# Optimization experiments

Hardware: AMD Instinct MI355X
Metric: run time of the kernel (lower is better)

The kernel has to match this reference:

```python
import jax, jax.numpy as jnp
import numpy as np

D_MODEL = 2048
N_HEADS = 16
D_HEAD = D_MODEL // N_HEADS
B, S = 4, 2048


def setup_inputs() -> dict:
    key = jax.random.key(0)
    ks = jax.random.split(key, 5)
    scale = 1.0 / np.sqrt(D_MODEL)
    return {
        "x": jax.random.normal(ks[0], (B, S, D_MODEL), dtype=jnp.float32),
        "w_qkv": jax.random.normal(ks[1], (D_MODEL, 3 * D_MODEL), dtype=jnp.float32) * scale,
        "b_qkv": jax.random.normal(ks[2], (3 * D_MODEL,), dtype=jnp.float32) * 0.01,
        "w_out": jax.random.normal(ks[3], (D_MODEL, D_MODEL), dtype=jnp.float32) * scale,
        "b_out": jax.random.normal(ks[4], (D_MODEL,), dtype=jnp.float32) * 0.01,
    }


def reference(x, w_qkv, b_qkv, w_out, b_out):
    b, s, d = x.shape
    qkv = x @ w_qkv + b_qkv                      # [b, s, 3d]
    q, k, v = jnp.split(qkv, 3, axis=-1)
    # [b, h, s, dh]
    q = q.reshape(b, s, N_HEADS, D_HEAD).transpose(0, 2, 1, 3)
    k = k.reshape(b, s, N_HEADS, D_HEAD).transpose(0, 2, 1, 3)
    v = v.reshape(b, s, N_HEADS, D_HEAD).transpose(0, 2, 1, 3)
    # past_kv is None -> s_past == s
    scale = 1.0 / np.sqrt(D_HEAD).astype(np.float32)
    scores = jnp.einsum("bhqd,bhkd->bhqk", q, k) * scale  # [b, h, s, s]
    # causal mask: disallow j > i (diagonal = 1 + s_past - s = 1)
    causal = jnp.tril(jnp.ones((s, s), dtype=bool))
    scores = jnp.where(causal, scores, jnp.float32(-jnp.inf))
    attn = jax.nn.softmax(scores, axis=-1)
    out = jnp.einsum("bhqk,bhkd->bhqd", attn, v)          # [b, h, s, dh]
    out = out.transpose(0, 2, 1, 3).reshape(b, s, d)
    out = out @ w_out + b_out
    return out, k, v
```

## Files before the change

### kernel.cpp

```cpp
#include <hip/hip_runtime.h>
#include <hip/hip_bf16.h>
#include <cstdint>

typedef unsigned short u16;
typedef unsigned int u32;
typedef __attribute__((ext_vector_type(4))) float f32x4;
typedef __attribute__((ext_vector_type(8))) __bf16 bf16x8;

#define DEVFN static __device__ __forceinline__

constexpr int Bb = 4, S = 2048, Dm = 2048, H = 16, DH = 128;
constexpr int M  = Bb * S;
constexpr int N3 = 3 * Dm;
constexpr float ATTN_SCALE = 0.088388347648318447f;
constexpr float LOG2E = 1.4426950408889634f;

DEVFN u16 f2bf(float f) {
  union { float f; u32 u; } v; v.f = f;
  u32 u = v.u;
  return (u16)((u + 0x7fffu + ((u >> 16) & 1u)) >> 16);
}

DEVFN void async16(const void* g, void* l) {
  __builtin_amdgcn_global_load_lds(
      (__attribute__((address_space(1))) unsigned int*)(g),
      (__attribute__((address_space(3))) unsigned int*)(l), 16, 0, 0);
}


__global__ __launch_bounds__(256) void k_cvt_bf16(const float* __restrict__ in,
                                                  u16* __restrict__ out, int n) {
  int i = (blockIdx.x * 256 + threadIdx.x) * 4;
  if (i < n) {
    float4 f = *(const float4*)(in + i);
    ushort4 o;
    o.x = f2bf(f.x); o.y = f2bf(f.y); o.z = f2bf(f.z); o.w = f2bf(f.w);
    *(ushort4*)(out + i) = o;
  }
}

__global__ __launch_bounds__(256) void k_transpose_bf16(const float* __restrict__ in,
                                                        u16* __restrict__ out,
                                                        int R, int C) {
  __shared__ float tile[32][33];
  int c0 = blockIdx.x * 32, r0 = blockIdx.y * 32;
  int tx = threadIdx.x & 31, ty = threadIdx.x >> 5;
#pragma unroll
  for (int i = 0; i < 4; i++)
    tile[ty + 8 * i][tx] = in[(size_t)(r0 + ty + 8 * i) * C + c0 + tx];
  __syncthreads();
#pragma unroll
  for (int i = 0; i < 4; i++)
    out[(size_t)(c0 + ty + 8 * i) * R + r0 + tx] = f2bf(tile[tx][ty + 8 * i]);
}


#define RA(buf, half) ((buf) * 65536 + (half) * 16384)
#define RB(buf, half) ((buf) * 65536 + 32768 + (half) * 16384)

DEVFN void stage_half(const u16* __restrict__ g, int grow0, int K, int vtile,
                      char* lds, int region, int tid) {
#pragma unroll
  for (int j = 0; j < 2; j++) {
    int L = j * 8192 + tid * 16;
    int row = L >> 7;
    int col = (((L & 127) ^ ((row & 7) << 4)) >> 1) + vtile * 64;
    async16(g + (size_t)(grow0 + row) * K + col,
            lds + region + j * 8192 + (tid & ~63) * 16);
  }
}

template <int BUF, int MSUB>
DEVFN void ldA(const char* lds, int wm, int lrow, int lkg, bf16x8 af[4][2]) {
#pragma unroll
  for (int mi = 0; mi < 4; mi++)
#pragma unroll
    for (int kk = 0; kk < 2; kk++) {
      int row = MSUB * 64 + mi * 16 + lrow;
      af[mi][kk] = *(const bf16x8*)(lds + RA(BUF, 0) + wm * 16384 + row * 128 +
                                    ((kk * 64 + lkg * 16) ^ ((row & 7) << 4)));
    }
}

template <int BUF, int NSUB>
DEVFN void ldB(const char* lds, int wn, int lrow, int lkg, bf16x8 bfr[2][2]) {
#pragma unroll
  for (int ni = 0; ni < 2; ni++)
#pragma unroll
    for (int kk = 0; kk < 2; kk++) {
      int row = (wn & 1) * 64 + NSUB * 32 + ni * 16 + lrow;
      bfr[ni][kk] = *(const bf16x8*)(lds + RB(BUF, 0) + (wn >> 1) * 16384 +
                                     row * 128 +
                                     ((kk * 64 + lkg * 16) ^ ((row & 7) << 4)));
    }
}

template <int MSUB, int NSUB>
DEVFN void mmq(f32x4 acc[8][4], bf16x8 af[4][2], bf16x8 bfr[2][2]) {
  __builtin_amdgcn_s_setprio(1);
#pragma unroll
  for (int kk = 0; kk < 2; kk++)
#pragma unroll
    for (int mi = 0; mi < 4; mi++)
#pragma unroll
      for (int ni = 0; ni < 2; ni++)
        acc[MSUB * 4 + mi][NSUB * 2 + ni] = __builtin_amdgcn_mfma_f32_16x16x32_bf16(
            af[mi][kk], bfr[ni][kk], acc[MSUB * 4 + mi][NSUB * 2 + ni], 0, 0, 0);
  __builtin_amdgcn_s_setprio(0);
}

#define BARRIER() __builtin_amdgcn_s_barrier()
#define LGK0() asm volatile("s_waitcnt lgkmcnt(0)" ::: "memory")
#define VM4() asm volatile("s_waitcnt vmcnt(4)" ::: "memory")

template <int MODE>
__global__ __launch_bounds__(512, 2) void k_gemm(
    const u16* __restrict__ A, const u16* __restrict__ BT,
    const float* __restrict__ bias, float* __restrict__ Cf,
    u16* __restrict__ q_bf, u16* __restrict__ k_bf, u16* __restrict__ v_bfT,
    int K, int N) {
  __shared__ __align__(16) char lds[131072];
  const int tid = threadIdx.x;
  const int wid = tid >> 6, lane = tid & 63;
  const int wm = wid >> 2, wn = wid & 3;
  const int lrow = lane & 15, lkg = lane >> 4;

  const int nbx = N >> 8;
  const int cpx = gridDim.x >> 3;
  const int wg = (blockIdx.x & 7) * cpx + (blockIdx.x >> 3);
  const int tm0 = (wg / nbx) << 8, tn0 = (wg % nbx) << 8;

  const int NT = K >> 6;

  f32x4 acc[8][4] = {};

  stage_half(A, tm0,       K, 0, lds, RA(0, 0), tid);
  stage_half(BT, tn0,      K, 0, lds, RB(0, 0), tid);
  stage_half(A, tm0 + 128, K, 0, lds, RA(0, 1), tid);
  stage_half(BT, tn0 + 128,K, 0, lds, RB(0, 1), tid);
  stage_half(A, tm0,       K, 1, lds, RA(1, 0), tid);
  stage_half(BT, tn0,      K, 1, lds, RB(1, 0), tid);
  VM4();
  BARRIER();

  for (int u = 0; u < NT; u += 2) {
    const int v2 = (u + 2 < NT) ? u + 2 : 0;
    const int v3 = (u + 3 < NT) ? u + 3 : 0;
    bf16x8 af[4][2], b0[2][2], b1[2][2];

    ldA<0, 0>(lds, wm, lrow, lkg, af);
    ldB<0, 0>(lds, wn, lrow, lkg, b0);
    stage_half(BT, tn0 + 128, K, u + 1, lds, RB(1, 1), tid);
    BARRIER(); LGK0();
    mmq<0, 0>(acc, af, b0);
    BARRIER();

    ldB<0, 1>(lds, wn, lrow, lkg, b1);
    stage_half(A, tm0 + 128, K, u + 1, lds, RA(1, 1), tid);
    BARRIER(); LGK0();
    mmq<0, 1>(acc, af, b1);
    BARRIER();

    ldA<0, 1>(lds, wm, lrow, lkg, af);
    stage_half(BT, tn0, K, v2, lds, RB(0, 0), tid);
    BARRIER(); LGK0();
    mmq<1, 0>(acc, af, b0);
    BARRIER();

    stage_half(A, tm0, K, v2, lds, RA(0, 0), tid);
    VM4();
    BARRIER();
    mmq<1, 1>(acc, af, b1);
    BARRIER();

    ldA<1, 0>(lds, wm, lrow, lkg, af);
    ldB<1, 0>(lds, wn, lrow, lkg, b0);
    stage_half(A, tm0 + 128, K, v2, lds, RA(0, 1), tid);
    BARRIER(); LGK0();
    mmq<0, 0>(acc, af, b0);
    BARRIER();

    ldB<1, 1>(lds, wn, lrow, lkg, b1);
    stage_half(BT, tn0 + 128, K, v2, lds, RB(0, 1), tid);
    BARRIER(); LGK0();
    mmq<0, 1>(acc, af, b1);
    BARRIER();

    ldA<1, 1>(lds, wm, lrow, lkg, af);
    stage_half(BT, tn0, K, v3, lds, RB(1, 0), tid);
    BARRIER(); LGK0();
    mmq<1, 0>(acc, af, b0);
    BARRIER();

    stage_half(A, tm0, K, v3, lds, RA(1, 0), tid);
    VM4();
    BARRIER();
    mmq<1, 1>(acc, af, b1);
    BARRIER();
  }

  if (MODE == 0) {
#pragma unroll
    for (int mig = 0; mig < 8; mig++) {
      int row = tm0 + wm * 128 + (mig >> 2) * 64 + (mig & 3) * 16 + lkg * 4;
#pragma unroll
      for (int nig = 0; nig < 4; nig++) {
        int col = tn0 + wn * 64 + (nig >> 1) * 32 + (nig & 1) * 16 + lrow;
        float bv = bias[col];
#pragma unroll
        for (int r = 0; r < 4; r++)
          Cf[(size_t)(row + r) * N + col] = acc[mig][nig][r] + bv;
      }
    }
  } else {
#pragma unroll
    for (int mig = 0; mig < 8; mig++) {
      int row = tm0 + wm * 128 + (mig >> 2) * 64 + (mig & 3) * 16 + lkg * 4;
#pragma unroll
      for (int nig = 0; nig < 4; nig++) {
        int n = tn0 + wn * 64 + (nig >> 1) * 32 + (nig & 1) * 16 + lrow;
        float bv = bias[n];
        int type = n >> 11;
        int d = n & 2047;
        int h = d >> 7, dh = d & 127;
#pragma unroll
        for (int r = 0; r < 4; r++) {
          int rr = row + r;
          int b = rr >> 11, s = rr & 2047;
          float val = acc[mig][nig][r] + bv;
          size_t idx = ((size_t)(b * H + h) * S + s) * DH + dh;
          if (type == 0) {
            q_bf[idx] = f2bf(val * ATTN_SCALE);
          } else if (type == 1) {
            Cf[(size_t)M * Dm + idx] = val;
            k_bf[idx] = f2bf(val);
          } else {
            Cf[(size_t)2 * M * Dm + idx] = val;
            v_bfT[((size_t)(b * H + h) * DH + dh) * S + s] = f2bf(val);
          }
        }
      }
    }
  }
}

__global__ __launch_bounds__(256, 2) void k_attn(const u16* __restrict__ q_bf,
                                                 const u16* __restrict__ k_bf,
                                                 const u16* __restrict__ v_bfT,
                                                 u16* __restrict__ attn_bf) {
  __shared__ u16 ldsK[64 * 128];
  __shared__ u16 ldsV[128 * 64];
  __shared__ u16 ldsP[4][32 * 64];

  const int tid = threadIdx.x;
  const int wid = tid >> 6, lane = tid & 63;
  const int lrow = lane & 15, lkg = lane >> 4;
  const int bh = blockIdx.y;
  const int b = bh >> 4, h = bh & 15;
  const int qi = 15 - blockIdx.x;
  const int qb0 = qi * 128;
  const int wq0 = qb0 + wid * 32;
  const int swz = (lrow & 7) << 4;

  const u16* qp = q_bf + (size_t)bh * S * DH;
  const u16* kp = k_bf + (size_t)bh * S * DH;
  const u16* vp = v_bfT + (size_t)bh * DH * S;

  bf16x8 qf[2][4];
#pragma unroll
  for (int qt = 0; qt < 2; qt++)
#pragma unroll
    for (int kk = 0; kk < 4; kk++)
      qf[qt][kk] = *(const bf16x8*)(qp + (size_t)(wq0 + qt * 16 + lrow) * DH +
                                    kk * 32 + lkg * 8);

  float mr[2][4], lr[2][4];
#pragma unroll
  for (int qt = 0; qt < 2; qt++)
#pragma unroll
    for (int r = 0; r < 4; r++) { mr[qt][r] = -1e30f; lr[qt][r] = 0.f; }
  f32x4 oacc[2][8] = {};

  const int nkb = qi * 2 + 2;

  for (int kb = 0; kb < nkb; kb++) {
    __syncthreads();
#pragma unroll
    for (int i = 0; i < 4; i++) {
      int L = i * 4096 + wid * 1024 + lane * 16;
      int krow = L >> 8, kch = (L >> 4) & 15;
      async16(kp + (size_t)(kb * 64 + krow) * DH + ((kch ^ (krow & 7)) * 8),
              (char*)ldsK + L);
      int vd = L >> 7, vch = (L >> 4) & 7;
      async16(vp + (size_t)vd * S + kb * 64 + ((vch ^ (vd & 7)) * 8),
              (char*)ldsV + L);
    }
    __syncthreads();

    if (kb * 64 <= wq0 + 31) {
      f32x4 sacc[2][4] = {};
#pragma unroll
      for (int kt = 0; kt < 4; kt++)
#pragma unroll
        for (int kk = 0; kk < 4; kk++) {
          bf16x8 kf = *(const bf16x8*)((const char*)ldsK +
                        (kt * 16 + lrow) * 256 + ((kk * 64 + lkg * 16) ^ swz));
          sacc[0][kt] = __builtin_amdgcn_mfma_f32_16x16x32_bf16(qf[0][kk], kf,
                                                                sacc[0][kt], 0, 0, 0);
          sacc[1][kt] = __builtin_amdgcn_mfma_f32_16x16x32_bf16(qf[1][kk], kf,
                                                                sacc[1][kt], 0, 0, 0);
        }

      if (kb * 64 + 63 > wq0) {
#pragma unroll
        for (int qt = 0; qt < 2; qt++)
#pragma unroll
          for (int kt = 0; kt < 4; kt++) {
            int k = kb * 64 + kt * 16 + lrow;
#pragma unroll
            for (int r = 0; r < 4; r++)
              if (k > wq0 + qt * 16 + lkg * 4 + r) sacc[qt][kt][r] = -1e30f;
          }
      }

      float pm[2][4];
#pragma unroll
      for (int qt = 0; qt < 2; qt++)
#pragma unroll
        for (int r = 0; r < 4; r++)
          pm[qt][r] = fmaxf(fmaxf(sacc[qt][0][r], sacc[qt][1][r]),
                            fmaxf(sacc[qt][2][r], sacc[qt][3][r]));
#pragma unroll
      for (int off = 1; off < 16; off <<= 1)
#pragma unroll
        for (int qt = 0; qt < 2; qt++)
#pragma unroll
          for (int r = 0; r < 4; r++)
            pm[qt][r] = fmaxf(pm[qt][r], __shfl_xor(pm[qt][r], off, 64));

      float sc[2][4];
#pragma unroll
      for (int qt = 0; qt < 2; qt++)
#pragma unroll
        for (int r = 0; r < 4; r++) {
          float mn = fmaxf(mr[qt][r], pm[qt][r]);
          sc[qt][r] = exp2f((mr[qt][r] - mn) * LOG2E);
          mr[qt][r] = mn;
        }

      float rs[2][4] = {};
#pragma unroll
      for (int qt = 0; qt < 2; qt++)
#pragma unroll
        for (int kt = 0; kt < 4; kt++)
#pragma unroll
          for (int r = 0; r < 4; r++) {
            float p = exp2f((sacc[qt][kt][r] - mr[qt][r]) * LOG2E);
            rs[qt][r] += p;
            int prow = qt * 16 + lkg * 4 + r;
            *(u16*)((char*)ldsP[wid] + prow * 128 +
                    (((kt * 16 + lrow) * 2) ^ ((prow & 7) << 4))) = f2bf(p);
          }
#pragma unroll
      for (int off = 1; off < 16; off <<= 1)
#pragma unroll
        for (int qt = 0; qt < 2; qt++)
#pragma unroll
          for (int r = 0; r < 4; r++)
            rs[qt][r] += __shfl_xor(rs[qt][r], off, 64);
#pragma unroll
      for (int qt = 0; qt < 2; qt++)
#pragma unroll
        for (int r = 0; r < 4; r++)
          lr[qt][r] = lr[qt][r] * sc[qt][r] + rs[qt][r];
#pragma unroll
      for (int qt = 0; qt < 2; qt++)
#pragma unroll
        for (int nd = 0; nd < 8; nd++)
#pragma unroll
          for (int r = 0; r < 4; r++) oacc[qt][nd][r] *= sc[qt][r];

      asm volatile("s_waitcnt lgkmcnt(0)" ::: "memory");
      bf16x8 pf[2][2];
#pragma unroll
      for (int qt = 0; qt < 2; qt++)
#pragma unroll
        for (int kk = 0; kk < 2; kk++)
          pf[qt][kk] = *(const bf16x8*)((const char*)ldsP[wid] +
                         (qt * 16 + lrow) * 128 + ((kk * 64 + lkg * 16) ^ swz));
#pragma unroll
      for (int nd = 0; nd < 8; nd++) {
        bf16x8 vf0 = *(const bf16x8*)((const char*)ldsV +
                       (nd * 16 + lrow) * 128 + ((lkg * 16) ^ swz));
        bf16x8 vf1 = *(const bf16x8*)((const char*)ldsV +
                       (nd * 16 + lrow) * 128 + ((64 + lkg * 16) ^ swz));
#pragma unroll
        for (int qt = 0; qt < 2; qt++) {
          oacc[qt][nd] = __builtin_amdgcn_mfma_f32_16x16x32_bf16(pf[qt][0], vf0,
                                                                 oacc[qt][nd], 0, 0, 0);
          oacc[qt][nd] = __builtin_amdgcn_mfma_f32_16x16x32_bf16(pf[qt][1], vf1,
                                                                 oacc[qt][nd], 0, 0, 0);
        }
      }
    }
  }

#pragma unroll
  for (int qt = 0; qt < 2; qt++) {
    float inv[4];
#pragma unroll
    for (int r = 0; r < 4; r++) inv[r] = 1.0f / lr[qt][r];
#pragma unroll
    for (int nd = 0; nd < 8; nd++)
#pragma unroll
      for (int r = 0; r < 4; r++) {
        int q = wq0 + qt * 16 + lkg * 4 + r;
        size_t idx = ((size_t)(b * S + q) * H + h) * DH + nd * 16 + lrow;
        attn_bf[idx] = f2bf(oacc[qt][nd][r] * inv[r]);
      }
  }
}


extern "C" void kernel_launch(void* const* d_in, const int* in_sizes, int n_in,
                              void* d_out, int out_size, void* d_ws, size_t ws_size,
                              hipStream_t stream) {
  const float* x     = (const float*)d_in[0];
  const float* w_qkv = (const float*)d_in[1];
  const float* b_qkv = (const float*)d_in[2];
  const float* w_out = (const float*)d_in[3];
  const float* b_out = (const float*)d_in[4];
  float* out = (float*)d_out;

  char* ws = (char*)d_ws;
  u16* x_bf    = (u16*)ws; ws += (size_t)M * Dm * 2;
  u16* wqkvT   = (u16*)ws; ws += (size_t)N3 * Dm * 2;
  u16* woutT   = (u16*)ws; ws += (size_t)Dm * Dm * 2;
  u16* q_bf    = (u16*)ws; ws += (size_t)M * Dm * 2;
  u16* k_bf    = (u16*)ws; ws += (size_t)M * Dm * 2;
  u16* v_bfT   = (u16*)ws; ws += (size_t)M * Dm * 2;
  u16* attn_bf = (u16*)ws; ws += (size_t)M * Dm * 2;

  k_cvt_bf16<<<(M * Dm) / 1024, 256, 0, stream>>>(x, x_bf, M * Dm);
  k_transpose_bf16<<<dim3(N3 / 32, Dm / 32), 256, 0, stream>>>(w_qkv, wqkvT, Dm, N3);
  k_transpose_bf16<<<dim3(Dm / 32, Dm / 32), 256, 0, stream>>>(w_out, woutT, Dm, Dm);

  k_gemm<1><<<(N3 / 256) * (M / 256), 512, 0, stream>>>(
      x_bf, wqkvT, b_qkv, out, q_bf, k_bf, v_bfT, Dm, N3);

  k_attn<<<dim3(S / 128, Bb * H), 256, 0, stream>>>(q_bf, k_bf, v_bfT, attn_bf);

  k_gemm<0><<<(Dm / 256) * (M / 256), 512, 0, stream>>>(
      attn_bf, woutT, b_out, out, nullptr, nullptr, nullptr, Dm, Dm);
}
```

Measured before the change: 640.7 us.

## Double-buffer K/V tiles in attention, add lazy rescaling and MFMA priority

The attention kernel now keeps two K/V LDS buffers and prefetches the next key block asynchronously while computing the current one. This replaces the two barriers per iteration with one wait-and-barrier at the end. It also skips the running-max update and the output/sum rescaling when the max grows by no more than a threshold, wavefront-wide (FA4-style lazy rescale). It raises wave priority around the MFMA sections. LDS use doubles for K/V, which may lower occupancy at 2 blocks/CU, and the lazy rescale lets exponentials grow up to e^8 before they are renormalised.

```diff
diff --git a/kernel.cpp b/kernel.cpp
--- a/kernel.cpp
+++ b/kernel.cpp
@@ -248,8 +248,8 @@
                                                  const u16* __restrict__ k_bf,
                                                  const u16* __restrict__ v_bfT,
                                                  u16* __restrict__ attn_bf) {
-  __shared__ u16 ldsK[64 * 128];
-  __shared__ u16 ldsV[128 * 64];
+  __shared__ u16 ldsK[2][64 * 128];
+  __shared__ u16 ldsV[2][128 * 64];
   __shared__ u16 ldsP[4][32 * 64];
 
   const int tid = threadIdx.x;
@@ -258,8 +258,7 @@
   const int bh = blockIdx.y;
   const int b = bh >> 4, h = bh & 15;
   const int qi = 15 - blockIdx.x;
-  const int qb0 = qi * 128;
-  const int wq0 = qb0 + wid * 32;
+  const int wq0 = qi * 128 + wid * 32;
   const int swz = (lrow & 7) << 4;
 
   const u16* qp = q_bf + (size_t)bh * S * DH;
@@ -283,33 +282,44 @@
 
   const int nkb = qi * 2 + 2;
 
-  for (int kb = 0; kb < nkb; kb++) {
-    __syncthreads();
+  auto stage = [&](int kb, int buf) {
 #pragma unroll
     for (int i = 0; i < 4; i++) {
       int L = i * 4096 + wid * 1024 + lane * 16;
       int krow = L >> 8, kch = (L >> 4) & 15;
       async16(kp + (size_t)(kb * 64 + krow) * DH + ((kch ^ (krow & 7)) * 8),
-              (char*)ldsK + L);
+              (char*)ldsK[buf] + L);
       int vd = L >> 7, vch = (L >> 4) & 7;
       async16(vp + (size_t)vd * S + kb * 64 + ((vch ^ (vd & 7)) * 8),
-              (char*)ldsV + L);
-    }
-    __syncthreads();
+              (char*)ldsV[buf] + L);
+    }
+  };
+
+  stage(0, 0);
+  asm volatile("s_waitcnt vmcnt(0)" ::: "memory");
+  __builtin_amdgcn_s_barrier();
+
+  int cur = 0;
+  for (int kb = 0; kb < nkb; kb++) {
+    if (kb + 1 < nkb) stage(kb + 1, cur ^ 1);
 
     if (kb * 64 <= wq0 + 31) {
+      const u16* Kc = ldsK[cur];
+      const u16* Vc = ldsV[cur];
       f32x4 sacc[2][4] = {};
+      __builtin_amdgcn_s_setprio(1);
 #pragma unroll
       for (int kt = 0; kt < 4; kt++)
 #pragma unroll
         for (int kk = 0; kk < 4; kk++) {
-          bf16x8 kf = *(const bf16x8*)((const char*)ldsK +
+          bf16x8 kf = *(const bf16x8*)((const char*)Kc +
                         (kt * 16 + lrow) * 256 + ((kk * 64 + lkg * 16) ^ swz));
           sacc[0][kt] = __builtin_amdgcn_mfma_f32_16x16x32_bf16(qf[0][kk], kf,
                                                                 sacc[0][kt], 0, 0, 0);
           sacc[1][kt] = __builtin_amdgcn_mfma_f32_16x16x32_bf16(qf[1][kk], kf,
                                                                 sacc[1][kt], 0, 0, 0);
         }
+      __builtin_amdgcn_s_setprio(0);
 
       if (kb * 64 + 63 > wq0) {
 #pragma unroll
@@ -338,15 +348,30 @@
           for (int r = 0; r < 4; r++)
             pm[qt][r] = fmaxf(pm[qt][r], __shfl_xor(pm[qt][r], off, 64));
 
-      float sc[2][4];
+      float dmax = pm[0][0] - mr[0][0];
 #pragma unroll
       for (int qt = 0; qt < 2; qt++)
 #pragma unroll
-        for (int r = 0; r < 4; r++) {
-          float mn = fmaxf(mr[qt][r], pm[qt][r]);
-          sc[qt][r] = exp2f((mr[qt][r] - mn) * LOG2E);
-          mr[qt][r] = mn;
-        }
+        for (int r = 0; r < 4; r++)
+          dmax = fmaxf(dmax, pm[qt][r] - mr[qt][r]);
+      if (!__all(dmax <= 8.0f)) {
+        float sc[2][4];
+#pragma unroll
+        for (int qt = 0; qt < 2; qt++)
+#pragma unroll
+          for (int r = 0; r < 4; r++) {
+            float mn = fmaxf(mr[qt][r], pm[qt][r]);
+            sc[qt][r] = exp2f((mr[qt][r] - mn) * LOG2E);
+            mr[qt][r] = mn;
+            lr[qt][r] *= sc[qt][r];
+          }
+#pragma unroll
+        for (int qt = 0; qt < 2; qt++)
+#pragma unroll
+          for (int nd = 0; nd < 8; nd++)
+#pragma unroll
+            for (int r = 0; r < 4; r++) oacc[qt][nd][r] *= sc[qt][r];
+      }
 
       float rs[2][4] = {};
 #pragma unroll
@@ -372,13 +397,7 @@
       for (int qt = 0; qt < 2; qt++)
 #pragma unroll
         for (int r = 0; r < 4; r++)
-          lr[qt][r] = lr[qt][r] * sc[qt][r] + rs[qt][r];
-#pragma unroll
-      for (int qt = 0; qt < 2; qt++)
-#pragma unroll
-        for (int nd = 0; nd < 8; nd++)
-#pragma unroll
-          for (int r = 0; r < 4; r++) oacc[qt][nd][r] *= sc[qt][r];
+          lr[qt][r] += rs[qt][r];
 
       asm volatile("s_waitcnt lgkmcnt(0)" ::: "memory");
       bf16x8 pf[2][2];
@@ -388,11 +407,12 @@
         for (int kk = 0; kk < 2; kk++)
           pf[qt][kk] = *(const bf16x8*)((const char*)ldsP[wid] +
                          (qt * 16 + lrow) * 128 + ((kk * 64 + lkg * 16) ^ swz));
+      __builtin_amdgcn_s_setprio(1);
 #pragma unroll
       for (int nd = 0; nd < 8; nd++) {
-        bf16x8 vf0 = *(const bf16x8*)((const char*)ldsV +
+        bf16x8 vf0 = *(const bf16x8*)((const char*)Vc +
                        (nd * 16 + lrow) * 128 + ((lkg * 16) ^ swz));
-        bf16x8 vf1 = *(const bf16x8*)((const char*)ldsV +
+        bf16x8 vf1 = *(const bf16x8*)((const char*)Vc +
                        (nd * 16 + lrow) * 128 + ((64 + lkg * 16) ^ swz));
 #pragma unroll
         for (int qt = 0; qt < 2; qt++) {
@@ -402,7 +422,12 @@
                                                                  oacc[qt][nd], 0, 0, 0);
         }
       }
-    }
+      __builtin_amdgcn_s_setprio(0);
+    }
+
+    asm volatile("s_waitcnt vmcnt(0)" ::: "memory");
+    __builtin_amdgcn_s_barrier();
+    cur ^= 1;
   }
 
 #pragma unroll
```

New measurement: 601.6 us. 6.1% less time.
